# Performance work log

Hardware: AMD Instinct MI355X
Metric: run time of the kernel (lower is better)

## Reference

```python
import jax, jax.numpy as jnp
import numpy as np

D_POINTS = 256
D_MODEL = 512
B, N = 8, 2048


def setup_inputs() -> dict:
    key = jax.random.key(0)
    ks = jax.random.split(key, 6)
    s_in = 1.0 / np.sqrt(D_POINTS)
    s_mid = 1.0 / np.sqrt(D_MODEL)
    return {
        "features": jax.random.normal(ks[0], (B, N, D_POINTS), dtype=jnp.float32),
        "Wq": jax.random.uniform(ks[1], (D_POINTS, D_MODEL), jnp.float32, -s_in, s_in),
        "Wk": jax.random.uniform(ks[2], (D_POINTS, D_MODEL), jnp.float32, -s_in, s_in),
        "Wv": jax.random.uniform(ks[3], (D_POINTS, D_MODEL), jnp.float32, -s_in, s_in),
        "W2": jax.random.uniform(ks[4], (D_MODEL, D_POINTS), jnp.float32, -s_mid, s_mid),
        "b2": jax.random.uniform(ks[5], (D_POINTS,), jnp.float32, -s_mid, s_mid),
    }


def reference(features, Wq, Wk, Wv, W2, b2):
    # features: [B, N, d_points]
    q = jnp.einsum("bnd,dm->bnm", features, Wq)  # [B, N, d_model]
    k = jnp.einsum("bnd,dm->bnm", features, Wk)
    v = jnp.einsum("bnd,dm->bnm", features, Wv)
    scale = 1.0 / np.sqrt(k.shape[-1]).astype(np.float32)
    attn = jax.nn.softmax(jnp.einsum("bnm,bkm->bnk", q, k) * scale, axis=-1)  # [B, N, N]
    res = jnp.einsum("bnk,bkm->bnm", attn, v)  # [B, N, d_model]
    res = jnp.einsum("bnm,md->bnd", res, W2) + b2  # fc2 -> [B, N, d_points]
    res = jax.nn.leaky_relu(res, negative_slope=0.2)
    return res + features
```

## Files before the change

### kernel.cpp

```cpp
#include <hip/hip_runtime.h>
#include <cstdint>

#define NBATCH 8
#define NSEQ   2048
#define NROWS  16384

typedef __attribute__((ext_vector_type(4))) float  f32x4;
typedef __attribute__((ext_vector_type(8))) short  short8;
typedef __attribute__((ext_vector_type(8))) __bf16 bf16x8;
typedef __attribute__((ext_vector_type(8))) _Float16 h8;

#define XB_OFF   0ul
#define WALL_OFF 8388608ul
#define Q_OFF    9175040ul
#define K_OFF    25952256ul
#define VT_OFF   42729472ul
#define W2T_OFF  59506688ul
#define O_OFF    59768832ul
#define RS_OFF   76546048ul
#define S_OFF    76611584ul

#define SCALE_Q 0.063758746f
#define FIXMAX  12.0f

__device__ __forceinline__ unsigned short f2bf(float f) {
  unsigned u = __builtin_bit_cast(unsigned, f);
  return (unsigned short)((u + 0x7fffu + ((u >> 16) & 1u)) >> 16);
}

__device__ __forceinline__ f32x4 mfma16(short8 a, short8 b, f32x4 c) {
  return __builtin_amdgcn_mfma_f32_16x16x32_bf16(
      __builtin_bit_cast(bf16x8, a), __builtin_bit_cast(bf16x8, b), c, 0, 0, 0);
}

__device__ __forceinline__ void glds16(const void* g, void* l) {
  __builtin_amdgcn_global_load_lds(
      (const __attribute__((address_space(1))) void*)g,
      (__attribute__((address_space(3))) void*)l, 16, 0, 0);
}

#define BAR_SYNC()                     \
  {                                    \
    __builtin_amdgcn_sched_barrier(0); \
    __builtin_amdgcn_s_barrier();      \
    __builtin_amdgcn_sched_barrier(0); \
  }
#define BAR_LGKM()                                           \
  {                                                          \
    asm volatile("s_waitcnt lgkmcnt(0)" ::: "memory");       \
    __builtin_amdgcn_sched_barrier(0);                       \
    __builtin_amdgcn_s_barrier();                            \
    __builtin_amdgcn_sched_barrier(0);                       \
  }
#define BAR_ALL()                                                    \
  {                                                                  \
    asm volatile("s_waitcnt vmcnt(0) lgkmcnt(0)" ::: "memory");      \
    __builtin_amdgcn_sched_barrier(0);                               \
    __builtin_amdgcn_s_barrier();                                    \
    __builtin_amdgcn_sched_barrier(0);                               \
  }
#define WAITV(N)                                                  \
  {                                                               \
    __builtin_amdgcn_sched_barrier(0);                            \
    asm volatile("s_waitcnt vmcnt(" #N ")" ::: "memory");         \
    __builtin_amdgcn_sched_barrier(0);                            \
  }

__global__ __launch_bounds__(256, 4) void prep_kernel(
    const float* __restrict__ feat, const float* __restrict__ Wq,
    const float* __restrict__ Wk, const float* __restrict__ Wv,
    const float* __restrict__ W2, char* __restrict__ ws) {
  int tid = blockIdx.x * 256 + threadIdx.x;
  if (tid < 524288) {
    int r = tid >> 5, co = (tid & 31) * 8;
    const float* src = feat + (size_t)r * 256 + co;
    short8 v;
#pragma unroll
    for (int i = 0; i < 8; ++i) v[i] = (short)f2bf(src[i]);
    unsigned short* Xb = (unsigned short*)(ws + XB_OFF);
    *(short8*)(Xb + (size_t)r * 256 + (co ^ ((r & 7) << 3))) = v;
  } else if (tid < 917504) {
    int t2 = tid - 524288;
    int m = t2 >> 8, d = t2 & 255;
    int wsel = m >> 9, mm = m & 511;
    const float* W = (wsel == 0) ? Wq : ((wsel == 1) ? Wk : Wv);
    float v = W[(size_t)d * 512 + mm];
    if (wsel == 0) v *= SCALE_Q;
    unsigned short* Wall = (unsigned short*)(ws + WALL_OFF);
    Wall[(size_t)m * 256 + (d ^ ((m & 7) << 3))] = f2bf(v);
  } else {
    int t3 = tid - 917504;
    int d = t3 >> 9, c = t3 & 511;
    int r = d & 127;
    size_t addr = (size_t)((d >> 7) * 8 + (c >> 6)) * 16384 + (size_t)r * 128 +
                  (size_t)((((c >> 3) & 7) ^ (r & 7)) * 16) + (c & 7) * 2;
    *(unsigned short*)(ws + W2T_OFF + addr) = f2bf(W2[(size_t)c * 256 + d]);
  }
}

__global__ __launch_bounds__(256, 2) void proj_kernel(char* __restrict__ ws) {
  __shared__ char smem[65536];
  const int tid = threadIdx.x;
  const int l = tid & 63, w = tid >> 6;
  const int g = l >> 4, m16 = l & 15;
  const int orig = blockIdx.x;
  const int wgid = (orig & 7) * 192 + (orig >> 3);
  const int nt = wgid % 12, mtb = wgid / 12;
  const char* XbT = ws + XB_OFF + (size_t)mtb * 65536;
  const char* WallT = ws + WALL_OFF + (size_t)nt * 65536;

  auto stage = [&](int buf, int kt) {
#pragma unroll
    for (int j = 0; j < 4; ++j) {
      int idx = j * 256 + tid;
      int r = idx >> 3, p = idx & 7;
      glds16(XbT + r * 512 + kt * 128 + p * 16, smem + buf * 16384 + idx * 16);
      glds16(WallT + r * 512 + kt * 128 + p * 16,
             smem + 32768 + buf * 16384 + idx * 16);
    }
  };

  const int mr = (w >> 1) * 64, nr = (w & 1) * 64;
  const int fxor = (m16 & 7) << 4;
  const f32x4 fz = {0.f, 0.f, 0.f, 0.f};
  f32x4 acc[4][4];
#pragma unroll
  for (int i = 0; i < 4; ++i)
#pragma unroll
    for (int j = 0; j < 4; ++j) acc[i][j] = fz;

  stage(0, 0);
  BAR_ALL();
#pragma unroll 1
  for (int kt = 0; kt < 4; ++kt) {
    if (kt < 3) stage((kt + 1) & 1, kt + 1);
    const char* Ab = smem + (kt & 1) * 16384;
    const char* Bb = smem + 32768 + (kt & 1) * 16384;
#pragma unroll
    for (int ks = 0; ks < 2; ++ks) {
      int off = (16 * g + 64 * ks) ^ fxor;
      short8 af[4], bf[4];
#pragma unroll
      for (int i = 0; i < 4; ++i)
        af[i] = *(const short8*)(Ab + (mr + i * 16 + m16) * 128 + off);
#pragma unroll
      for (int i = 0; i < 4; ++i)
        bf[i] = *(const short8*)(Bb + (nr + i * 16 + m16) * 128 + off);
#pragma unroll
      for (int mi = 0; mi < 4; ++mi)
#pragma unroll
        for (int ni = 0; ni < 4; ++ni)
          acc[mi][ni] = mfma16(af[mi], bf[ni], acc[mi][ni]);
    }
    BAR_ALL();
  }

  const int colg = nt * 128 + nr;
  const int tcat = colg >> 9;
  const int cin_base = colg & 511;
  char* wbuf = smem + w * 2048;
  if (tcat < 2) {
    char* dst = ws + (tcat == 0 ? Q_OFF : K_OFF) +
                ((size_t)(mtb * 8 + (cin_base >> 6))) * 16384;
#pragma unroll
    for (int mi = 0; mi < 4; ++mi) {
#pragma unroll
      for (int ni = 0; ni < 4; ++ni)
#pragma unroll
        for (int j = 0; j < 4; ++j) {
          int r = g * 4 + j, c = ni * 16 + m16;
          *(unsigned short*)(wbuf + r * 128 + ((2 * c) ^ ((r & 7) << 4))) =
              f2bf(acc[mi][ni][j]);
        }
      asm volatile("s_waitcnt lgkmcnt(0)" ::: "memory");
      __builtin_amdgcn_sched_barrier(0);
#pragma unroll
      for (int s = 0; s < 2; ++s) {
        int cid = l + 64 * s;
        int r2 = cid >> 3, gi = cid & 7;
        short8 v = *(const short8*)(wbuf + r2 * 128 + gi * 16);
        int rt = mr + mi * 16 + r2;
        *(short8*)(dst + (size_t)rt * 128 + gi * 16) = v;
      }
    }
  } else {
    int cin = cin_base + l;
    int grow0 = mtb * 128 + mr;
    int z2 = grow0 >> 11;
    int k0 = (grow0 & 2047) >> 5;
    char* vbase = ws + VT_OFF + (size_t)z2 * 2097152 +
                  (size_t)(cin >> 6) * 4096 + (size_t)((cin >> 4) & 3) * 1024 +
                  (size_t)(cin & 15) * 16;
#pragma unroll
    for (int mi = 0; mi < 4; ++mi) {
#pragma unroll
      for (int ni = 0; ni < 4; ++ni)
#pragma unroll
        for (int j = 0; j < 4; ++j) {
          int r = g * 4 + j, c = ni * 16 + m16;
          *(unsigned short*)(wbuf + r * 128 + ((2 * c) ^ ((r & 7) << 4))) =
              f2bf(acc[mi][ni][j]);
        }
      asm volatile("s_waitcnt lgkmcnt(0)" ::: "memory");
      __builtin_amdgcn_sched_barrier(0);
      unsigned short vals[16];
#pragma unroll
      for (int r2 = 0; r2 < 16; ++r2)
        vals[r2] = *(const unsigned short*)(wbuf + r2 * 128 +
                                            ((2 * l) ^ ((r2 & 7) << 4)));
      short8 v0, v1;
#pragma unroll
      for (int i2 = 0; i2 < 8; ++i2) {
        v0[i2] = (short)vals[i2];
        v1[i2] = (short)vals[8 + i2];
      }
      int kt32 = k0 + (mi >> 1);
      int gb = (mi & 1) * 2;
      *(short8*)(vbase + (size_t)kt32 * 32768 + gb * 256) = v0;
      *(short8*)(vbase + (size_t)kt32 * 32768 + (gb + 1) * 256) = v1;
    }
  }
}

__global__ __launch_bounds__(256, 2) void qk_kernel(
    const char* __restrict__ ws, char* __restrict__ Sb, int nb, int b0) {
  __shared__ char smem[65536];
  const int tid = threadIdx.x;
  const int bid = blockIdx.x;
  const int z = bid % nb, tile = bid / nb;
  const int mt = tile >> 4, ntq = tile & 15;
  const int b = b0 + z;
  const int l = tid & 63, w = tid >> 6;
  const int g = l >> 4, m16 = l & 15;
  const int fxor = (m16 & 7) << 4;
  const char* Qt = ws + Q_OFF + (size_t)(b * 16 + mt) * 131072;
  const char* Kt = ws + K_OFF + (size_t)(b * 16 + ntq) * 131072;

  auto stage = [&](int buf, int kt) {
#pragma unroll
    for (int j = 0; j < 4; ++j) {
      int idx = j * 256 + tid;
      glds16(Qt + (size_t)kt * 16384 + idx * 16, smem + buf * 16384 + idx * 16);
      glds16(Kt + (size_t)kt * 16384 + idx * 16,
             smem + 32768 + buf * 16384 + idx * 16);
    }
  };

  const int mr = (w >> 1) * 64, nr = (w & 1) * 64;
  const f32x4 fz = {0.f, 0.f, 0.f, 0.f};
  f32x4 acc[4][4];
#pragma unroll
  for (int i = 0; i < 4; ++i)
#pragma unroll
    for (int j = 0; j < 4; ++j) acc[i][j] = fz;

  stage(0, 0);
  BAR_ALL();
#pragma unroll 1
  for (int kt = 0; kt < 8; ++kt) {
    if (kt < 7) stage((kt + 1) & 1, kt + 1);
    const char* Ab = smem + (kt & 1) * 16384;
    const char* Bb = smem + 32768 + (kt & 1) * 16384;
#pragma unroll
    for (int ks = 0; ks < 2; ++ks) {
      int off = (16 * g + 64 * ks) ^ fxor;
      short8 af[4], bf[4];
#pragma unroll
      for (int i = 0; i < 4; ++i)
        af[i] = *(const short8*)(Ab + (mr + i * 16 + m16) * 128 + off);
#pragma unroll
      for (int i = 0; i < 4; ++i)
        bf[i] = *(const short8*)(Bb + (nr + i * 16 + m16) * 128 + off);
#pragma unroll
      for (int mi = 0; mi < 4; ++mi)
#pragma unroll
        for (int ni = 0; ni < 4; ++ni)
          acc[mi][ni] = mfma16(af[mi], bf[ni], acc[mi][ni]);
    }
    BAR_ALL();
  }

#pragma unroll
  for (int mi = 0; mi < 4; ++mi)
#pragma unroll
    for (int ni = 0; ni < 4; ++ni)
#pragma unroll
      for (int j = 0; j < 4; ++j) {
        int r = mr + mi * 16 + g * 4 + j, c = nr + ni * 16 + m16;
        *(unsigned short*)(smem + r * 272 + 2 * c) =
            __builtin_bit_cast(unsigned short, (_Float16)acc[mi][ni][j]);
      }
  BAR_LGKM();
  char* Sz = Sb + (size_t)z * 8388608;
#pragma unroll
  for (int it = 0; it < 8; ++it) {
    int idx = it * 256 + tid;
    int rgh = idx >> 10, rem = idx & 1023;
    int kt32L = rem >> 8, rem2 = rem & 255;
    int mi2 = rem2 >> 6, lslot = rem2 & 63;
    int row = rgh * 64 + mi2 * 16 + (lslot & 15);
    int bcol = kt32L * 64 + (lslot >> 4) * 16;
    short8 v = *(const short8*)(smem + row * 272 + bcol);
    *(short8*)(Sz + (size_t)(mt * 2 + rgh) * 262144 +
               (size_t)(ntq * 4 + kt32L) * 4096 + mi2 * 1024 + lslot * 16) = v;
  }
}

__global__ __launch_bounds__(256, 2) void stats_kernel(
    char* __restrict__ Sb, float* __restrict__ rs_out, int nb, int b0) {
  const int tid = threadIdx.x;
  const int bid = blockIdx.x;
  const int z = bid % nb, rg = bid / nb;
  char* R = Sb + (size_t)z * 8388608 + (size_t)rg * 262144;
  float sum = 0.f;
#pragma unroll 4
  for (int i = 0; i < 64; ++i) {
    char* p = R + ((size_t)i * 256 + tid) * 16;
    h8 hv = *(const h8*)p;
    short8 pk;
#pragma unroll
    for (int j = 0; j < 8; ++j) {
      float e = exp2f((float)hv[j] - FIXMAX);
      sum += e;
      pk[j] = (short)f2bf(e);
    }
    *(short8*)p = pk;
  }
  sum += __shfl_xor(sum, 16);
  sum += __shfl_xor(sum, 32);
  if ((tid & 48) == 0) {
    int myrow = ((tid >> 6) & 3) * 16 + (tid & 15);
    rs_out[(size_t)(b0 + z) * 2048 + rg * 64 + myrow] = 1.0f / sum;
  }
}

__global__ __launch_bounds__(256, 2) void pv_kernel(
    char* __restrict__ ws, char* __restrict__ Sb, int nb, int b0) {
  __shared__ char smem[32768];
  const int tid = threadIdx.x;
  const int bid = blockIdx.x;
  const int z = bid % nb, tile = bid / nb;
  const int cb = tile & 1, mt64 = tile >> 1;
  const int b = b0 + z;
  const int l = tid & 63, w = tid >> 6;
  const int g = l >> 4, m16 = l & 15;
  const char* Pr = Sb + (size_t)z * 8388608 + (size_t)mt64 * 262144;
  const char* Vt = ws + VT_OFF + (size_t)b * 2097152 + (size_t)cb * 16384;

  const f32x4 fz = {0.f, 0.f, 0.f, 0.f};
  f32x4 acc[4][4];
#pragma unroll
  for (int i = 0; i < 4; ++i)
#pragma unroll
    for (int j = 0; j < 4; ++j) acc[i][j] = fz;

  auto loadP = [&](short8(&pf)[4], int kt) {
    const char* p = Pr + (size_t)kt * 4096 + l * 16;
#pragma unroll
    for (int mi = 0; mi < 4; ++mi)
      pf[mi] = *(const short8*)(p + mi * 1024);
  };
  auto stageV = [&](int buf, int kt) {
#pragma unroll
    for (int j = 0; j < 4; ++j) {
      int idx = j * 256 + tid;
      glds16(Vt + (size_t)kt * 32768 + idx * 16, smem + buf * 16384 + idx * 16);
    }
  };
  auto compute = [&](int buf, short8(&pf)[4]) {
    const char* Vb = smem + buf * 16384 + w * 4096 + l * 16;
    short8 vf[4];
#pragma unroll
    for (int ni = 0; ni < 4; ++ni) vf[ni] = *(const short8*)(Vb + ni * 1024);
#pragma unroll
    for (int mi = 0; mi < 4; ++mi)
#pragma unroll
      for (int ni = 0; ni < 4; ++ni)
        acc[mi][ni] = mfma16(pf[mi], vf[ni], acc[mi][ni]);
  };

  short8 pA[4], pB[4];
  loadP(pA, 0);
  stageV(0, 0);
  WAITV(0);
  BAR_SYNC();
#pragma unroll 1
  for (int kt2 = 0; kt2 < 32; ++kt2) {
    const int kt = kt2 * 2;
    loadP(pB, kt + 1);
    stageV(1, kt + 1);
    WAITV(8);
    BAR_SYNC();
    compute(0, pA);
    BAR_LGKM();
    if (kt + 2 < 64) {
      loadP(pA, kt + 2);
      stageV(0, kt + 2);
      WAITV(8);
    } else {
      WAITV(0);
    }
    BAR_SYNC();
    compute(1, pB);
    BAR_LGKM();
  }

  const float* rsp = (const float*)(ws + RS_OFF) + (size_t)b * 2048 + mt64 * 64;
#pragma unroll
  for (int mi = 0; mi < 4; ++mi) {
    f32x4 rv;
#pragma unroll
    for (int j = 0; j < 4; ++j) rv[j] = rsp[mi * 16 + g * 4 + j];
#pragma unroll
    for (int ni = 0; ni < 4; ++ni) acc[mi][ni] *= rv;
  }
  char* wbuf = smem + w * 2048;
  const int tI = b * 16 + (mt64 >> 1);
  char* dst = ws + O_OFF + ((size_t)tI * 8 + cb * 4 + w) * 16384 +
              (size_t)(mt64 & 1) * 8192;
#pragma unroll 1
  for (int mi = 0; mi < 4; ++mi) {
#pragma unroll
    for (int ni = 0; ni < 4; ++ni)
#pragma unroll
      for (int j = 0; j < 4; ++j) {
        int r = g * 4 + j, c = ni * 16 + m16;
        *(unsigned short*)(wbuf + r * 128 + ((2 * c) ^ ((r & 7) << 4))) =
            f2bf(acc[mi][ni][j]);
      }
    asm volatile("s_waitcnt lgkmcnt(0)" ::: "memory");
    __builtin_amdgcn_sched_barrier(0);
#pragma unroll
    for (int s = 0; s < 2; ++s) {
      int cid = l + 64 * s;
      int r2 = cid >> 3, gi = cid & 7;
      short8 v = *(const short8*)(wbuf + r2 * 128 + gi * 16);
      *(short8*)(dst + (size_t)(mi * 16 + r2) * 128 + gi * 16) = v;
    }
  }
}

__global__ __launch_bounds__(256, 2) void fc2_kernel(
    const char* __restrict__ ws, const float* __restrict__ feat,
    const float* __restrict__ b2, float* __restrict__ out) {
  __shared__ char smem[65536];
  const int tid = threadIdx.x;
  const int mtF = blockIdx.x >> 1, ntF = blockIdx.x & 1;
  const int l = tid & 63, w = tid >> 6;
  const int g = l >> 4, m16 = l & 15;
  const int fxor = (m16 & 7) << 4;
  const char* At = ws + O_OFF + (size_t)mtF * 131072;
  const char* Bt = ws + W2T_OFF + (size_t)ntF * 131072;

  auto stage = [&](int buf, int kt) {
#pragma unroll
    for (int j = 0; j < 4; ++j) {
      int idx = j * 256 + tid;
      glds16(At + (size_t)kt * 16384 + idx * 16, smem + buf * 16384 + idx * 16);
      glds16(Bt + (size_t)kt * 16384 + idx * 16,
             smem + 32768 + buf * 16384 + idx * 16);
    }
  };

  const int mr = (w >> 1) * 64, nr = (w & 1) * 64;
  const f32x4 fz = {0.f, 0.f, 0.f, 0.f};
  f32x4 acc[4][4];
#pragma unroll
  for (int i = 0; i < 4; ++i)
#pragma unroll
    for (int j = 0; j < 4; ++j) acc[i][j] = fz;

  stage(0, 0);
  BAR_ALL();
#pragma unroll 1
  for (int kt = 0; kt < 8; ++kt) {
    if (kt < 7) stage((kt + 1) & 1, kt + 1);
    const char* Ab = smem + (kt & 1) * 16384;
    const char* Bb = smem + 32768 + (kt & 1) * 16384;
#pragma unroll
    for (int ks = 0; ks < 2; ++ks) {
      int off = (16 * g + 64 * ks) ^ fxor;
      short8 af[4], bf[4];
#pragma unroll
      for (int i = 0; i < 4; ++i)
        af[i] = *(const short8*)(Ab + (mr + i * 16 + m16) * 128 + off);
#pragma unroll
      for (int i = 0; i < 4; ++i)
        bf[i] = *(const short8*)(Bb + (nr + i * 16 + m16) * 128 + off);
#pragma unroll
      for (int mi = 0; mi < 4; ++mi)
#pragma unroll
        for (int ni = 0; ni < 4; ++ni)
          acc[mi][ni] = mfma16(af[mi], bf[ni], acc[mi][ni]);
    }
    BAR_ALL();
  }

#pragma unroll
  for (int mi = 0; mi < 4; ++mi)
#pragma unroll
    for (int ni = 0; ni < 4; ++ni) {
      int d = ntF * 128 + nr + ni * 16 + m16;
      float bias = b2[d];
#pragma unroll
      for (int j = 0; j < 4; ++j) {
        size_t m = (size_t)mtF * 128 + mr + mi * 16 + g * 4 + j;
        float v = acc[mi][ni][j] + bias;
        v = v > 0.f ? v : 0.2f * v;
        out[m * 256 + d] = v + feat[m * 256 + d];
      }
    }
}

extern "C" void kernel_launch(void* const* d_in, const int* in_sizes, int n_in,
                              void* d_out, int out_size, void* d_ws, size_t ws_size,
                              hipStream_t stream) {
  const float* feat = (const float*)d_in[0];
  const float* Wq = (const float*)d_in[1];
  const float* Wk = (const float*)d_in[2];
  const float* Wv = (const float*)d_in[3];
  const float* W2 = (const float*)d_in[4];
  const float* b2 = (const float*)d_in[5];
  float* out = (float*)d_out;
  char* ws = (char*)d_ws;
  (void)in_sizes; (void)n_in; (void)out_size;

  prep_kernel<<<4096, 256, 0, stream>>>(feat, Wq, Wk, Wv, W2, ws);
  proj_kernel<<<1536, 256, 0, stream>>>(ws);

  const size_t per_batch = 8388608ul;
  int nb = 8;
  while (nb > 1 && S_OFF + (size_t)nb * per_batch > ws_size) nb >>= 1;
  char* Sb = ws + S_OFF;
  float* rs = (float*)(ws + RS_OFF);
  for (int b0 = 0; b0 < 8; b0 += nb) {
    qk_kernel<<<256 * nb, 256, 0, stream>>>(ws, Sb, nb, b0);
    stats_kernel<<<32 * nb, 256, 0, stream>>>(Sb, rs, nb, b0);
    pv_kernel<<<64 * nb, 256, 0, stream>>>(ws, Sb, nb, b0);
  }
  fc2_kernel<<<256, 256, 0, stream>>>(ws, feat, b2, out);
}
```

Measured before the change: 177.4 us.

## Widen PV tiles to all 512 columns and split stats rows across blocks

The PV kernel now runs 512 threads per block and covers all 512 value columns, so each P tile is read once instead of twice. Each stage takes a K step of 64 with 128KB of LDS double buffering, and some per-stage LGKM barriers are folded into the vmcnt waits. The stats kernel splits each 64-row group into four 16-row blocks and reduces through shared memory, giving four times as many blocks for better occupancy. The larger LDS footprint and fewer PV blocks (256 in total) may limit occupancy and latency hiding.

```diff
diff --git a/kernel.cpp b/kernel.cpp
--- a/kernel.cpp
+++ b/kernel.cpp
@@ -59,11 +59,11 @@
     __builtin_amdgcn_s_barrier();                                    \
     __builtin_amdgcn_sched_barrier(0);                               \
   }
-#define WAITV(N)                                                  \
-  {                                                               \
-    __builtin_amdgcn_sched_barrier(0);                            \
-    asm volatile("s_waitcnt vmcnt(" #N ")" ::: "memory");         \
-    __builtin_amdgcn_sched_barrier(0);                            \
+#define WAITVL(N)                                                         \
+  {                                                                       \
+    __builtin_amdgcn_sched_barrier(0);                                    \
+    asm volatile("s_waitcnt vmcnt(" #N ") lgkmcnt(0)" ::: "memory");      \
+    __builtin_amdgcn_sched_barrier(0);                                    \
   }
 
 __global__ __launch_bounds__(256, 4) void prep_kernel(
@@ -306,16 +306,19 @@
   }
 }
 
-__global__ __launch_bounds__(256, 2) void stats_kernel(
+__global__ __launch_bounds__(256, 4) void stats_kernel(
     char* __restrict__ Sb, float* __restrict__ rs_out, int nb, int b0) {
   const int tid = threadIdx.x;
   const int bid = blockIdx.x;
-  const int z = bid % nb, rg = bid / nb;
-  char* R = Sb + (size_t)z * 8388608 + (size_t)rg * 262144;
+  const int z = bid % nb, rem = bid / nb;
+  const int rg = rem >> 2, mi = rem & 3;
+  char* Base = Sb + (size_t)z * 8388608 + (size_t)rg * 262144 + mi * 1024;
   float sum = 0.f;
 #pragma unroll 4
-  for (int i = 0; i < 64; ++i) {
-    char* p = R + ((size_t)i * 256 + tid) * 16;
+  for (int i = 0; i < 16; ++i) {
+    int idx = i * 256 + tid;
+    int kt32 = idx >> 6, l2 = idx & 63;
+    char* p = Base + (size_t)kt32 * 4096 + l2 * 16;
     h8 hv = *(const h8*)p;
     short8 pk;
 #pragma unroll
@@ -328,24 +331,27 @@
   }
   sum += __shfl_xor(sum, 16);
   sum += __shfl_xor(sum, 32);
-  if ((tid & 48) == 0) {
-    int myrow = ((tid >> 6) & 3) * 16 + (tid & 15);
-    rs_out[(size_t)(b0 + z) * 2048 + rg * 64 + myrow] = 1.0f / sum;
-  }
-}
-
-__global__ __launch_bounds__(256, 2) void pv_kernel(
+  __shared__ float red[4][16];
+  const int w = tid >> 6, l = tid & 63;
+  if (l < 16) red[w][l] = sum;
+  __syncthreads();
+  if (tid < 16) {
+    float s = red[0][tid] + red[1][tid] + red[2][tid] + red[3][tid];
+    rs_out[(size_t)(b0 + z) * 2048 + rg * 64 + mi * 16 + tid] = 1.0f / s;
+  }
+}
+
+__global__ __launch_bounds__(512, 2) void pv_kernel(
     char* __restrict__ ws, char* __restrict__ Sb, int nb, int b0) {
-  __shared__ char smem[32768];
+  __shared__ char smem[131072];
   const int tid = threadIdx.x;
   const int bid = blockIdx.x;
-  const int z = bid % nb, tile = bid / nb;
-  const int cb = tile & 1, mt64 = tile >> 1;
+  const int z = bid % nb, mt64 = bid / nb;
   const int b = b0 + z;
   const int l = tid & 63, w = tid >> 6;
   const int g = l >> 4, m16 = l & 15;
   const char* Pr = Sb + (size_t)z * 8388608 + (size_t)mt64 * 262144;
-  const char* Vt = ws + VT_OFF + (size_t)b * 2097152 + (size_t)cb * 16384;
+  const char* Vt = ws + VT_OFF + (size_t)b * 2097152;
 
   const f32x4 fz = {0.f, 0.f, 0.f, 0.f};
   f32x4 acc[4][4];
@@ -354,56 +360,66 @@
 #pragma unroll
     for (int j = 0; j < 4; ++j) acc[i][j] = fz;
 
-  auto loadP = [&](short8(&pf)[4], int kt) {
-    const char* p = Pr + (size_t)kt * 4096 + l * 16;
-#pragma unroll
-    for (int mi = 0; mi < 4; ++mi)
-      pf[mi] = *(const short8*)(p + mi * 1024);
+  auto loadP = [&](short8(&pf)[8], int kt) {
+    const char* p = Pr + (size_t)kt * 8192 + l * 16;
+#pragma unroll
+    for (int s = 0; s < 2; ++s)
+#pragma unroll
+      for (int mi = 0; mi < 4; ++mi)
+        pf[s * 4 + mi] = *(const short8*)(p + s * 4096 + mi * 1024);
   };
   auto stageV = [&](int buf, int kt) {
 #pragma unroll
-    for (int j = 0; j < 4; ++j) {
-      int idx = j * 256 + tid;
-      glds16(Vt + (size_t)kt * 32768 + idx * 16, smem + buf * 16384 + idx * 16);
+    for (int j = 0; j < 8; ++j) {
+      int idx = j * 512 + tid;
+      glds16(Vt + (size_t)kt * 65536 + idx * 16,
+             smem + buf * 65536 + idx * 16);
     }
   };
-  auto compute = [&](int buf, short8(&pf)[4]) {
-    const char* Vb = smem + buf * 16384 + w * 4096 + l * 16;
-    short8 vf[4];
-#pragma unroll
-    for (int ni = 0; ni < 4; ++ni) vf[ni] = *(const short8*)(Vb + ni * 1024);
-#pragma unroll
-    for (int mi = 0; mi < 4; ++mi)
+  auto compute = [&](int buf, short8(&pf)[8]) {
+    const char* Vb = smem + buf * 65536 + w * 4096 + l * 16;
+#pragma unroll
+    for (int s = 0; s < 2; ++s) {
+      short8 vf[4];
 #pragma unroll
       for (int ni = 0; ni < 4; ++ni)
-        acc[mi][ni] = mfma16(pf[mi], vf[ni], acc[mi][ni]);
+        vf[ni] = *(const short8*)(Vb + s * 32768 + ni * 1024);
+#pragma unroll
+      for (int mi = 0; mi < 4; ++mi)
+#pragma unroll
+        for (int ni = 0; ni < 4; ++ni)
+          acc[mi][ni] = mfma16(pf[s * 4 + mi], vf[ni], acc[mi][ni]);
+    }
   };
 
-  short8 pA[4], pB[4];
+  short8 pA[8], pB[8];
   loadP(pA, 0);
   stageV(0, 0);
-  WAITV(0);
+  WAITVL(0);
   BAR_SYNC();
 #pragma unroll 1
-  for (int kt2 = 0; kt2 < 32; ++kt2) {
+  for (int kt2 = 0; kt2 < 16; ++kt2) {
     const int kt = kt2 * 2;
-    loadP(pB, kt + 1);
-    stageV(1, kt + 1);
-    WAITV(8);
+    if (kt + 1 < 32) {
+      loadP(pB, kt + 1);
+      stageV(1, kt + 1);
+      WAITVL(16);
+    } else {
+      WAITVL(0);
+    }
     BAR_SYNC();
     compute(0, pA);
-    BAR_LGKM();
-    if (kt + 2 < 64) {
+    if (kt + 2 < 32) {
       loadP(pA, kt + 2);
       stageV(0, kt + 2);
-      WAITV(8);
+      WAITVL(16);
     } else {
-      WAITV(0);
+      WAITVL(0);
     }
     BAR_SYNC();
     compute(1, pB);
-    BAR_LGKM();
-  }
+  }
+  BAR_ALL();
 
   const float* rsp = (const float*)(ws + RS_OFF) + (size_t)b * 2048 + mt64 * 64;
 #pragma unroll
@@ -415,8 +431,7 @@
     for (int ni = 0; ni < 4; ++ni) acc[mi][ni] *= rv;
   }
   char* wbuf = smem + w * 2048;
-  const int tI = b * 16 + (mt64 >> 1);
-  char* dst = ws + O_OFF + ((size_t)tI * 8 + cb * 4 + w) * 16384 +
+  char* dst = ws + O_OFF + ((size_t)(b * 16 + (mt64 >> 1)) * 8 + w) * 16384 +
               (size_t)(mt64 & 1) * 8192;
 #pragma unroll 1
   for (int mi = 0; mi < 4; ++mi) {
@@ -535,8 +550,8 @@
   float* rs = (float*)(ws + RS_OFF);
   for (int b0 = 0; b0 < 8; b0 += nb) {
     qk_kernel<<<256 * nb, 256, 0, stream>>>(ws, Sb, nb, b0);
-    stats_kernel<<<32 * nb, 256, 0, stream>>>(Sb, rs, nb, b0);
-    pv_kernel<<<64 * nb, 256, 0, stream>>>(ws, Sb, nb, b0);
+    stats_kernel<<<128 * nb, 256, 0, stream>>>(Sb, rs, nb, b0);
+    pv_kernel<<<32 * nb, 512, 0, stream>>>(ws, Sb, nb, b0);
   }
   fc2_kernel<<<256, 256, 0, stream>>>(ws, feat, b2, out);
 }
```

After: 177.0 us. About the same (-0.2%).
